# Performance work log

Measured on AMD Instinct MI355X. Metric: run time of the kernel, lower is better.

The kernel has to match this reference:

```python
import jax, jax.numpy as jnp
import numpy as np

B, L, D, H, E, V, TCAP = 64, 196, 512, 512, 512, 32000, 32


def setup_inputs() -> dict:
    key = jax.random.key(0)
    ks = jax.random.split(key, 12)
    s = 0.02  # small init scale for numerical stability
    return {
        "img_features": jax.random.normal(ks[0], (B, L, D), jnp.float32),
        "captions": jax.random.randint(ks[1], (B, TCAP), 0, V, jnp.int32),
        "embed_table": jax.random.normal(ks[2], (V, E), jnp.float32) * s,
        "W_feat": jax.random.normal(ks[3], (D, D), jnp.float32) * s,
        "W_h": jax.random.normal(ks[4], (H, D), jnp.float32) * s,
        "att_bias": jnp.zeros((L,), jnp.float32),
        "v_att": jax.random.normal(ks[5], (D,), jnp.float32) * s,
        "W_ih": jax.random.normal(ks[6], (4 * H, E + D), jnp.float32) * s,
        "W_hh": jax.random.normal(ks[7], (4 * H, H), jnp.float32) * s,
        "b_ih": jnp.zeros((4 * H,), jnp.float32),
        "b_hh": jnp.zeros((4 * H,), jnp.float32),
        "W_out": jax.random.normal(ks[8], (V, H), jnp.float32) * s,
        "b_out": jnp.zeros((V,), jnp.float32),
    }


def reference(img_features, captions, embed_table, W_feat, W_h, att_bias, v_att,
              W_ih, W_hh, b_ih, b_hh, W_out, b_out):
    # init states: mean over feature locations (D == H branch of initialize_states)
    mean_feat = img_features.mean(axis=1)            # [B, H]
    h0 = mean_feat
    c0 = mean_feat

    max_cap_len = captions.shape[1] - 1              # T
    word_emb = embed_table[captions]                 # [B, T+1, E] (no dropout: eval)
    emb_seq = jnp.swapaxes(word_emb[:, :max_cap_len, :], 0, 1)  # [T, B, E]

    # feature projection is h-independent -> hoist out of the loop
    feat_proj = jnp.einsum('bld,de->ble', img_features, W_feat)  # [B, L, D]

    def step(carry, emb_t):
        h, c = carry
        # Bahdanau attention: relu(W_feat f + W_h h + b) . v, softmax over L
        att = jax.nn.relu(feat_proj + (h @ W_h)[:, None, :] + att_bias[None, :, None])
        score = jnp.einsum('bld,d->bl', att, v_att)              # [B, L]
        alpha = jax.nn.softmax(score, axis=1)                    # [B, L]
        context = jnp.einsum('bl,bld->bd', alpha, img_features)  # [B, D]
        # LSTMCell (torch gate order: i, f, g, o)
        x = jnp.concatenate([emb_t, context], axis=1)            # [B, E+D]
        gates = x @ W_ih.T + b_ih + h @ W_hh.T + b_hh            # [B, 4H]
        i, f, g, o = jnp.split(gates, 4, axis=1)
        c_new = jax.nn.sigmoid(f) * c + jax.nn.sigmoid(i) * jnp.tanh(g)
        h_new = jax.nn.sigmoid(o) * jnp.tanh(c_new)
        out = h_new @ W_out.T + b_out                            # [B, V]
        return (h_new, c_new), (out, alpha)

    (_, _), (preds, alphas) = jax.lax.scan(step, (h0, c0), emb_seq)
    predictions = jnp.swapaxes(preds, 0, 1)   # [B, T, V]
    alphas = jnp.swapaxes(alphas, 0, 1)       # [B, T, L]
    return predictions, alphas
```

## Files before the change

### kernel.cpp

```cpp
#include <hip/hip_runtime.h>

typedef unsigned short u16;
typedef __attribute__((ext_vector_type(4))) float f32x4;
typedef __attribute__((ext_vector_type(8))) short short8;

#define B_ 64
#define L_ 196
#define D_ 512
#define T_ 31
#define V_ 32000

__device__ __forceinline__ float b2f(unsigned int u) {
    union { float f; unsigned int u; } x; x.u = u << 16; return x.f;
}
__device__ __forceinline__ u16 f2b(float f) {
    union { float f; unsigned int u; } x; x.f = f;
    unsigned int r = x.u + 0x7fffu + ((x.u >> 16) & 1u);
    return (u16)(r >> 16);
}
__device__ __forceinline__ void unpack8(uint4 v, float* f) {
    f[0] = b2f(v.x & 0xffffu); f[1] = b2f(v.x >> 16);
    f[2] = b2f(v.y & 0xffffu); f[3] = b2f(v.y >> 16);
    f[4] = b2f(v.z & 0xffffu); f[5] = b2f(v.z >> 16);
    f[6] = b2f(v.w & 0xffffu); f[7] = b2f(v.w >> 16);
}

__global__ __launch_bounds__(256) void convert_kernel(
        const float* __restrict__ src, u16* __restrict__ dst, int n4) {
    int i = blockIdx.x * 256 + threadIdx.x;
    if (i >= n4) return;
    float4 v = *(const float4*)(src + (size_t)i * 4);
    u16* d = dst + (size_t)i * 4;
    d[0] = f2b(v.x); d[1] = f2b(v.y); d[2] = f2b(v.z); d[3] = f2b(v.w);
}

__global__ __launch_bounds__(256) void prep_kernel(
        const float* __restrict__ Wfeat, const float* __restrict__ Wih,
        const float* __restrict__ Whh, const float* __restrict__ table,
        const int* __restrict__ cap,
        u16* __restrict__ WfT, u16* __restrict__ Wcat,
        u16* __restrict__ Wemb, u16* __restrict__ Aemb) {
    int idx = blockIdx.x * 256 + threadIdx.x;
    if (idx < 512 * 512) {
        WfT[idx] = f2b(Wfeat[(idx & 511) * 512 + (idx >> 9)]);
    }
    if (idx < 2048 * 1024) {
        int j = idx >> 10, k = idx & 1023;
        Wcat[idx] = f2b((k < 512) ? Wih[j * 1024 + 512 + k] : Whh[j * 512 + (k - 512)]);
    }
    if (idx < 2048 * 512) {
        int j = idx >> 9, k = idx & 511;
        Wemb[idx] = f2b(Wih[j * 1024 + k]);
    }
    if (idx < 1984 * 512) {
        int m = idx >> 9, k = idx & 511;
        int t = m >> 6, b = m & 63;
        Aemb[idx] = f2b(table[(size_t)cap[b * 32 + t] * 512 + k]);
    }
}

__global__ __launch_bounds__(512) void init_kernel(
        const float* __restrict__ img, const float* __restrict__ Wh,
        float* __restrict__ c, u16* __restrict__ xcat, float* __restrict__ hWh) {
    __shared__ float hl[512];
    int b = blockIdx.x, d = threadIdx.x;
    const float* p = img + (size_t)b * L_ * D_ + d;
    float s = 0.f;
    for (int l = 0; l < L_; l++) s += p[l * D_];
    float mean = s * (1.0f / 196.0f);
    c[b * 512 + d] = mean;
    xcat[b * 1024 + 512 + d] = f2b(mean);
    hl[d] = mean;
    __syncthreads();
    float acc = 0.f;
    const float* wp = Wh + d;
    for (int k = 0; k < 512; k++) acc += hl[k] * wp[k * 512];
    hWh[b * 512 + d] = acc;
}

__global__ __launch_bounds__(256) void score_kernel(
        const u16* __restrict__ fp, const float* __restrict__ hWh,
        const float* __restrict__ att_bias, const float* __restrict__ v_att,
        float* __restrict__ score) {
    int b = blockIdx.y;
    int l = blockIdx.x * 4 + (threadIdx.x >> 6);
    int lane = threadIdx.x & 63;
    uint4 fv = *(const uint4*)(fp + ((size_t)(b * L_ + l)) * D_ + lane * 8);
    float4 h0 = *(const float4*)(hWh + b * D_ + lane * 8);
    float4 h1 = *(const float4*)(hWh + b * D_ + lane * 8 + 4);
    float4 v0 = *(const float4*)(v_att + lane * 8);
    float4 v1 = *(const float4*)(v_att + lane * 8 + 4);
    float ab = att_bias[l];
    float f[8];
    unpack8(fv, f);
    float hh[8] = {h0.x, h0.y, h0.z, h0.w, h1.x, h1.y, h1.z, h1.w};
    float vv[8] = {v0.x, v0.y, v0.z, v0.w, v1.x, v1.y, v1.z, v1.w};
    float acc = 0.f;
#pragma unroll
    for (int j = 0; j < 8; j++) {
        float a = f[j] + hh[j] + ab;
        a = fmaxf(a, 0.f);
        acc += a * vv[j];
    }
#pragma unroll
    for (int off = 32; off; off >>= 1) acc += __shfl_xor(acc, off, 64);
    if (lane == 0) score[b * L_ + l] = acc;
}

__global__ __launch_bounds__(256) void softctx_kernel(
        const float* __restrict__ score, const float* __restrict__ img,
        float* __restrict__ alphas_out, u16* __restrict__ xcat, int t) {
    __shared__ float sl[256];
    __shared__ float al[196];
    int b = blockIdx.x, tid = threadIdx.x;
    float s = (tid < L_) ? score[b * L_ + tid] : -3.4e38f;
    sl[tid] = s;
    __syncthreads();
    for (int off = 128; off; off >>= 1) {
        if (tid < off) sl[tid] = fmaxf(sl[tid], sl[tid + off]);
        __syncthreads();
    }
    float mx = sl[0];
    __syncthreads();
    float e = (tid < L_) ? expf(s - mx) : 0.f;
    sl[tid] = e;
    __syncthreads();
    for (int off = 128; off; off >>= 1) {
        if (tid < off) sl[tid] += sl[tid + off];
        __syncthreads();
    }
    float inv = 1.f / sl[0];
    if (tid < L_) {
        float a = e * inv;
        al[tid] = a;
        alphas_out[((size_t)(b * T_ + t)) * L_ + tid] = a;
    }
    __syncthreads();
    float c0 = 0.f, c1 = 0.f;
    const float* ib = img + (size_t)b * L_ * D_;
    for (int l = 0; l < L_; l++) {
        float a = al[l];
        c0 += a * ib[l * D_ + tid];
        c1 += a * ib[l * D_ + tid + 256];
    }
    xcat[b * 1024 + tid] = f2b(c0);
    xcat[b * 1024 + tid + 256] = f2b(c1);
}

__global__ __launch_bounds__(256) void gates_kernel(
        const u16* __restrict__ xcat, const u16* __restrict__ Wcat,
        const float* __restrict__ gemb, const float* __restrict__ bih,
        const float* __restrict__ bhh, float* __restrict__ gates, int t) {
    __shared__ __align__(16) u16 At[16 * 40];
    __shared__ __align__(16) u16 Bt[64 * 40];
    int tid = threadIdx.x, wave = tid >> 6, lane = tid & 63;
    int m0 = blockIdx.y * 16, n0 = blockIdx.x * 64;
    f32x4 acc = {0.f, 0.f, 0.f, 0.f};
    int sr = tid >> 2, sc = (tid & 3) * 8;
    const u16* Ap = xcat + (size_t)(m0 + (sr & 15)) * 1024 + sc;
    const u16* Bp = Wcat + (size_t)(n0 + sr) * 1024 + sc;
    int fm = lane & 15, fk = (lane >> 4) * 8;
    for (int k0 = 0; k0 < 1024; k0 += 32) {
        uint4 av = {0, 0, 0, 0};
        uint4 bv = *(const uint4*)(Bp + k0);
        if (tid < 64) av = *(const uint4*)(Ap + k0);
        __syncthreads();
        if (tid < 64) *(uint4*)(&At[(sr & 15) * 40 + sc]) = av;
        *(uint4*)(&Bt[sr * 40 + sc]) = bv;
        __syncthreads();
        short8 a = *(const short8*)(&At[fm * 40 + fk]);
        short8 bb = *(const short8*)(&Bt[(wave * 16 + fm) * 40 + fk]);
        acc = __builtin_amdgcn_mfma_f32_16x16x32_bf16(a, bb, acc, 0, 0, 0);
    }
    int crow = (lane >> 4) * 4, ccol = n0 + wave * 16 + (lane & 15);
#pragma unroll
    for (int r = 0; r < 4; r++) {
        int row = m0 + crow + r;
        float v = acc[r] + gemb[((size_t)(t * 64 + row)) * 2048 + ccol]
                + bih[ccol] + bhh[ccol];
        gates[row * 2048 + ccol] = v;
    }
}

__global__ __launch_bounds__(512) void lstm_kernel(
        const float* __restrict__ gates, float* __restrict__ c,
        const float* __restrict__ Wh, u16* __restrict__ xcat,
        u16* __restrict__ hseq, float* __restrict__ hWh, int t) {
    __shared__ float hl[512];
    int b = blockIdx.x, d = threadIdx.x;
    const float* g = gates + b * 2048;
    float gi = g[d], gf = g[512 + d], gg = g[1024 + d], go = g[1536 + d];
    float cold = c[b * 512 + d];
    float si = 1.f / (1.f + expf(-gi));
    float sf = 1.f / (1.f + expf(-gf));
    float so = 1.f / (1.f + expf(-go));
    float cn = sf * cold + si * tanhf(gg);
    float hn = so * tanhf(cn);
    c[b * 512 + d] = cn;
    u16 hb = f2b(hn);
    xcat[b * 1024 + 512 + d] = hb;
    hseq[((size_t)(b * T_ + t)) * 512 + d] = hb;
    hl[d] = hn;
    __syncthreads();
    float acc = 0.f;
    const float* wp = Wh + d;
    for (int k = 0; k < 512; k++) acc += hl[k] * wp[k * 512];
    hWh[b * 512 + d] = acc;
}

template <int MODE>
__global__ __launch_bounds__(256) void gemm64_kernel(
        const u16* __restrict__ A, const u16* __restrict__ Bm,
        int lda, int ldb, int K, void* __restrict__ Cv, int ldc,
        const float* __restrict__ bias) {
    __shared__ __align__(16) u16 At[64 * 40];
    __shared__ __align__(16) u16 Bt[64 * 40];
    int tid = threadIdx.x, wave = tid >> 6, lane = tid & 63;
    int wm = (wave >> 1) * 32, wn = (wave & 1) * 32;
    size_t m0 = (size_t)blockIdx.y * 64, n0 = (size_t)blockIdx.x * 64;
    f32x4 acc[2][2];
#pragma unroll
    for (int i = 0; i < 2; i++)
#pragma unroll
        for (int j = 0; j < 2; j++) acc[i][j] = {0.f, 0.f, 0.f, 0.f};
    int sr = tid >> 2, sc = (tid & 3) * 8;
    const u16* Ap = A + (m0 + sr) * (size_t)lda + sc;
    const u16* Bp = Bm + (n0 + sr) * (size_t)ldb + sc;
    int fm = lane & 15, fk = (lane >> 4) * 8;
    for (int k0 = 0; k0 < K; k0 += 32) {
        uint4 av = *(const uint4*)(Ap + k0);
        uint4 bv = *(const uint4*)(Bp + k0);
        __syncthreads();
        *(uint4*)(&At[sr * 40 + sc]) = av;
        *(uint4*)(&Bt[sr * 40 + sc]) = bv;
        __syncthreads();
        short8 a0 = *(const short8*)(&At[(wm + fm) * 40 + fk]);
        short8 a1 = *(const short8*)(&At[(wm + 16 + fm) * 40 + fk]);
        short8 b0 = *(const short8*)(&Bt[(wn + fm) * 40 + fk]);
        short8 b1 = *(const short8*)(&Bt[(wn + 16 + fm) * 40 + fk]);
        acc[0][0] = __builtin_amdgcn_mfma_f32_16x16x32_bf16(a0, b0, acc[0][0], 0, 0, 0);
        acc[0][1] = __builtin_amdgcn_mfma_f32_16x16x32_bf16(a0, b1, acc[0][1], 0, 0, 0);
        acc[1][0] = __builtin_amdgcn_mfma_f32_16x16x32_bf16(a1, b0, acc[1][0], 0, 0, 0);
        acc[1][1] = __builtin_amdgcn_mfma_f32_16x16x32_bf16(a1, b1, acc[1][1], 0, 0, 0);
    }
    int crow = (lane >> 4) * 4, ccol = lane & 15;
#pragma unroll
    for (int mi = 0; mi < 2; mi++)
#pragma unroll
        for (int ni = 0; ni < 2; ni++)
#pragma unroll
            for (int r = 0; r < 4; r++) {
                size_t row = m0 + wm + mi * 16 + crow + r;
                size_t col = n0 + wn + ni * 16 + ccol;
                float v = acc[mi][ni][r];
                if (MODE == 0) {
                    ((u16*)Cv)[row * (size_t)ldc + col] = f2b(v);
                } else {
                    if (MODE == 1) v += bias[col];
                    ((float*)Cv)[row * (size_t)ldc + col] = v;
                }
            }
}

extern "C" void kernel_launch(void* const* d_in, const int* in_sizes, int n_in,
                              void* d_out, int out_size, void* d_ws, size_t ws_size,
                              hipStream_t stream) {
    (void)in_sizes; (void)n_in; (void)out_size; (void)ws_size;
    const float* img   = (const float*)d_in[0];
    const int*   cap   = (const int*)d_in[1];
    const float* table = (const float*)d_in[2];
    const float* Wf    = (const float*)d_in[3];
    const float* Wh    = (const float*)d_in[4];
    const float* ab    = (const float*)d_in[5];
    const float* va    = (const float*)d_in[6];
    const float* Wih   = (const float*)d_in[7];
    const float* Whh   = (const float*)d_in[8];
    const float* bih   = (const float*)d_in[9];
    const float* bhh   = (const float*)d_in[10];
    const float* Wout  = (const float*)d_in[11];
    const float* bout  = (const float*)d_in[12];

    float* dout = (float*)d_out;
    float* alph = dout + (size_t)B_ * T_ * V_;

    char* w = (char*)d_ws;
    u16*   imgb  = (u16*)(w);
    u16*   fpb   = (u16*)(w + 12845056);
    u16*   Woutb = (u16*)(w + 25690112);
    u16*   Wcat  = (u16*)(w + 58458112);
    u16*   Wemb  = (u16*)(w + 62652416);
    u16*   WfT   = (u16*)(w + 64749568);
    u16*   Aemb  = (u16*)(w + 65273856);
    u16*   hseq  = (u16*)(w + 67305472);
    float* gemb  = (float*)(w + 69337088);
    u16*   xcat  = (u16*)(w + 85590016);
    float* gates = (float*)(w + 85721088);
    float* score = (float*)(w + 86245376);
    float* hWh   = (float*)(w + 86295552);
    float* cbuf  = (float*)(w + 86426624);

    convert_kernel<<<6272, 256, 0, stream>>>(img, imgb, 12544 * 512 / 4);
    convert_kernel<<<16000, 256, 0, stream>>>(Wout, Woutb, 32000 * 512 / 4);
    prep_kernel<<<8192, 256, 0, stream>>>(Wf, Wih, Whh, table, cap, WfT, Wcat, Wemb, Aemb);
    gemm64_kernel<0><<<dim3(8, 196), 256, 0, stream>>>(imgb, WfT, 512, 512, 512, fpb, 512, nullptr);
    gemm64_kernel<2><<<dim3(32, 31), 256, 0, stream>>>(Aemb, Wemb, 512, 512, 512, gemb, 2048, nullptr);
    init_kernel<<<64, 512, 0, stream>>>(img, Wh, cbuf, xcat, hWh);

    for (int t = 0; t < T_; t++) {
        score_kernel<<<dim3(49, 64), 256, 0, stream>>>(fpb, hWh, ab, va, score);
        softctx_kernel<<<64, 256, 0, stream>>>(score, img, alph, xcat, t);
        gates_kernel<<<dim3(32, 4), 256, 0, stream>>>(xcat, Wcat, gemb, bih, bhh, gates, t);
        lstm_kernel<<<64, 512, 0, stream>>>(gates, cbuf, Wh, xcat, hseq, hWh, t);
    }

    gemm64_kernel<1><<<dim3(500, 31), 256, 0, stream>>>(hseq, Woutb, 512, 512, 512, dout, 32000, bout);
}
```

Baseline: 1.907 ms.

## Fuse recurrent timestep kernels into one persistent cooperative kernel with grid syncs

Replaces the four per-timestep kernel launches (score, softmax/context, gates GEMM, LSTM) with a single cooperative persistent kernel of 256 blocks that uses grid.sync between phases. Each phase is re-partitioned across more blocks, with split-K partial sums for the gates and split-D for context and the hWh projection, and the cell state is double-buffered. The intent is to remove launch overhead and idle GPU time across 124 tiny launches in exchange for grid-barrier cost. It also adds an XCD-aware block swizzle and nontemporal stores to the output-projection GEMM.

Measured after the change: 4.884 ms. 156% more time.

```diff
diff --git a/kernel.cpp b/kernel.cpp
--- a/kernel.cpp
+++ b/kernel.cpp
@@ -1,4 +1,7 @@
 #include <hip/hip_runtime.h>
+#include <hip/hip_cooperative_groups.h>
+
+namespace cg = cooperative_groups;
 
 typedef unsigned short u16;
 typedef __attribute__((ext_vector_type(4))) float f32x4;
@@ -78,137 +81,180 @@
     hWh[b * 512 + d] = acc;
 }
 
-__global__ __launch_bounds__(256) void score_kernel(
-        const u16* __restrict__ fp, const float* __restrict__ hWh,
-        const float* __restrict__ att_bias, const float* __restrict__ v_att,
-        float* __restrict__ score) {
-    int b = blockIdx.y;
-    int l = blockIdx.x * 4 + (threadIdx.x >> 6);
-    int lane = threadIdx.x & 63;
-    uint4 fv = *(const uint4*)(fp + ((size_t)(b * L_ + l)) * D_ + lane * 8);
-    float4 h0 = *(const float4*)(hWh + b * D_ + lane * 8);
-    float4 h1 = *(const float4*)(hWh + b * D_ + lane * 8 + 4);
-    float4 v0 = *(const float4*)(v_att + lane * 8);
-    float4 v1 = *(const float4*)(v_att + lane * 8 + 4);
-    float ab = att_bias[l];
-    float f[8];
-    unpack8(fv, f);
-    float hh[8] = {h0.x, h0.y, h0.z, h0.w, h1.x, h1.y, h1.z, h1.w};
-    float vv[8] = {v0.x, v0.y, v0.z, v0.w, v1.x, v1.y, v1.z, v1.w};
-    float acc = 0.f;
-#pragma unroll
-    for (int j = 0; j < 8; j++) {
-        float a = f[j] + hh[j] + ab;
-        a = fmaxf(a, 0.f);
-        acc += a * vv[j];
-    }
-#pragma unroll
-    for (int off = 32; off; off >>= 1) acc += __shfl_xor(acc, off, 64);
-    if (lane == 0) score[b * L_ + l] = acc;
-}
-
-__global__ __launch_bounds__(256) void softctx_kernel(
-        const float* __restrict__ score, const float* __restrict__ img,
-        float* __restrict__ alphas_out, u16* __restrict__ xcat, int t) {
+__global__ __launch_bounds__(512, 2) void loop_kernel(
+        const float* __restrict__ img,
+        const u16*   __restrict__ fpb,
+        const float* __restrict__ Wh,
+        const float* __restrict__ ab,
+        const float* __restrict__ va,
+        const u16*   __restrict__ Wcat,
+        const float* __restrict__ gemb,
+        const float* __restrict__ bih, const float* __restrict__ bhh,
+        u16*   __restrict__ xcat,
+        u16*   __restrict__ hseq,
+        float* __restrict__ score,
+        float* __restrict__ hWh,
+        float* __restrict__ c0b, float* __restrict__ c1b,
+        float* __restrict__ gpart,
+        float* __restrict__ alph) {
+    __shared__ __align__(16) u16 At[64 * 40];
+    __shared__ __align__(16) u16 Bt[64 * 40];
+    __shared__ float hl[512];
+    __shared__ float fbuf[512];
     __shared__ float sl[256];
     __shared__ float al[196];
-    int b = blockIdx.x, tid = threadIdx.x;
-    float s = (tid < L_) ? score[b * L_ + tid] : -3.4e38f;
-    sl[tid] = s;
-    __syncthreads();
-    for (int off = 128; off; off >>= 1) {
-        if (tid < off) sl[tid] = fmaxf(sl[tid], sl[tid + off]);
-        __syncthreads();
-    }
-    float mx = sl[0];
-    __syncthreads();
-    float e = (tid < L_) ? expf(s - mx) : 0.f;
-    sl[tid] = e;
-    __syncthreads();
-    for (int off = 128; off; off >>= 1) {
-        if (tid < off) sl[tid] += sl[tid + off];
-        __syncthreads();
-    }
-    float inv = 1.f / sl[0];
-    if (tid < L_) {
-        float a = e * inv;
-        al[tid] = a;
-        alphas_out[((size_t)(b * T_ + t)) * L_ + tid] = a;
-    }
-    __syncthreads();
-    float c0 = 0.f, c1 = 0.f;
-    const float* ib = img + (size_t)b * L_ * D_;
-    for (int l = 0; l < L_; l++) {
-        float a = al[l];
-        c0 += a * ib[l * D_ + tid];
-        c1 += a * ib[l * D_ + tid + 256];
-    }
-    xcat[b * 1024 + tid] = f2b(c0);
-    xcat[b * 1024 + tid + 256] = f2b(c1);
-}
-
-__global__ __launch_bounds__(256) void gates_kernel(
-        const u16* __restrict__ xcat, const u16* __restrict__ Wcat,
-        const float* __restrict__ gemb, const float* __restrict__ bih,
-        const float* __restrict__ bhh, float* __restrict__ gates, int t) {
-    __shared__ __align__(16) u16 At[16 * 40];
-    __shared__ __align__(16) u16 Bt[64 * 40];
-    int tid = threadIdx.x, wave = tid >> 6, lane = tid & 63;
-    int m0 = blockIdx.y * 16, n0 = blockIdx.x * 64;
-    f32x4 acc = {0.f, 0.f, 0.f, 0.f};
-    int sr = tid >> 2, sc = (tid & 3) * 8;
-    const u16* Ap = xcat + (size_t)(m0 + (sr & 15)) * 1024 + sc;
-    const u16* Bp = Wcat + (size_t)(n0 + sr) * 1024 + sc;
-    int fm = lane & 15, fk = (lane >> 4) * 8;
-    for (int k0 = 0; k0 < 1024; k0 += 32) {
-        uint4 av = {0, 0, 0, 0};
-        uint4 bv = *(const uint4*)(Bp + k0);
-        if (tid < 64) av = *(const uint4*)(Ap + k0);
-        __syncthreads();
-        if (tid < 64) *(uint4*)(&At[(sr & 15) * 40 + sc]) = av;
-        *(uint4*)(&Bt[sr * 40 + sc]) = bv;
-        __syncthreads();
-        short8 a = *(const short8*)(&At[fm * 40 + fk]);
-        short8 bb = *(const short8*)(&Bt[(wave * 16 + fm) * 40 + fk]);
-        acc = __builtin_amdgcn_mfma_f32_16x16x32_bf16(a, bb, acc, 0, 0, 0);
-    }
-    int crow = (lane >> 4) * 4, ccol = n0 + wave * 16 + (lane & 15);
-#pragma unroll
-    for (int r = 0; r < 4; r++) {
-        int row = m0 + crow + r;
-        float v = acc[r] + gemb[((size_t)(t * 64 + row)) * 2048 + ccol]
-                + bih[ccol] + bhh[ccol];
-        gates[row * 2048 + ccol] = v;
-    }
-}
-
-__global__ __launch_bounds__(512) void lstm_kernel(
-        const float* __restrict__ gates, float* __restrict__ c,
-        const float* __restrict__ Wh, u16* __restrict__ xcat,
-        u16* __restrict__ hseq, float* __restrict__ hWh, int t) {
-    __shared__ float hl[512];
-    int b = blockIdx.x, d = threadIdx.x;
-    const float* g = gates + b * 2048;
-    float gi = g[d], gf = g[512 + d], gg = g[1024 + d], go = g[1536 + d];
-    float cold = c[b * 512 + d];
-    float si = 1.f / (1.f + expf(-gi));
-    float sf = 1.f / (1.f + expf(-gf));
-    float so = 1.f / (1.f + expf(-go));
-    float cn = sf * cold + si * tanhf(gg);
-    float hn = so * tanhf(cn);
-    c[b * 512 + d] = cn;
-    u16 hb = f2b(hn);
-    xcat[b * 1024 + 512 + d] = hb;
-    hseq[((size_t)(b * T_ + t)) * 512 + d] = hb;
-    hl[d] = hn;
-    __syncthreads();
-    float acc = 0.f;
-    const float* wp = Wh + d;
-    for (int k = 0; k < 512; k++) acc += hl[k] * wp[k * 512];
-    hWh[b * 512 + d] = acc;
-}
-
-template <int MODE>
+
+    cg::grid_group grid = cg::this_grid();
+    int bid = blockIdx.x;
+    int tid = threadIdx.x;
+    int lane = tid & 63;
+    int wv = tid >> 6;
+
+    for (int t = 0; t < T_; t++) {
+        {
+            int gw = bid * 8 + wv;
+            int b = gw >> 5;
+            int lw = gw & 31;
+            float4 h0 = *(const float4*)(hWh + b * 512 + lane * 8);
+            float4 h1 = *(const float4*)(hWh + b * 512 + lane * 8 + 4);
+            float4 v0 = *(const float4*)(va + lane * 8);
+            float4 v1 = *(const float4*)(va + lane * 8 + 4);
+            float hh[8] = {h0.x, h0.y, h0.z, h0.w, h1.x, h1.y, h1.z, h1.w};
+            float vv[8] = {v0.x, v0.y, v0.z, v0.w, v1.x, v1.y, v1.z, v1.w};
+            for (int l = lw; l < L_; l += 32) {
+                uint4 fv = *(const uint4*)(fpb + ((size_t)(b * L_ + l)) * 512 + lane * 8);
+                float f[8];
+                unpack8(fv, f);
+                float abl = ab[l];
+                float acc = 0.f;
+#pragma unroll
+                for (int j = 0; j < 8; j++) {
+                    float a = f[j] + hh[j] + abl;
+                    a = fmaxf(a, 0.f);
+                    acc += a * vv[j];
+                }
+#pragma unroll
+                for (int off = 32; off; off >>= 1) acc += __shfl_xor(acc, off, 64);
+                if (lane == 0) score[b * L_ + l] = acc;
+            }
+        }
+        grid.sync();
+        {
+            int b = bid >> 2, q = bid & 3;
+            float s = (tid < L_) ? score[b * L_ + tid] : -3.4e38f;
+            if (tid < 256) sl[tid] = s;
+            __syncthreads();
+            for (int off = 128; off; off >>= 1) {
+                if (tid < off) sl[tid] = fmaxf(sl[tid], sl[tid + off]);
+                __syncthreads();
+            }
+            float mx = sl[0];
+            __syncthreads();
+            float e = (tid < L_) ? expf(s - mx) : 0.f;
+            if (tid < 256) sl[tid] = e;
+            __syncthreads();
+            for (int off = 128; off; off >>= 1) {
+                if (tid < off) sl[tid] += sl[tid + off];
+                __syncthreads();
+            }
+            float inv = 1.f / sl[0];
+            if (tid < L_) {
+                float a = e * inv;
+                al[tid] = a;
+                if (q == 0) alph[((size_t)(b * T_ + t)) * L_ + tid] = a;
+            }
+            __syncthreads();
+            int dq = tid & 127, ls = tid >> 7;
+            const float* ib = img + (size_t)b * L_ * 512 + q * 128 + dq;
+            float cacc = 0.f;
+            for (int l = ls; l < L_; l += 4) cacc += al[l] * ib[(size_t)l * 512];
+            fbuf[tid] = cacc;
+            __syncthreads();
+            if (tid < 128) {
+                float v = fbuf[tid] + fbuf[tid + 128] + fbuf[tid + 256] + fbuf[tid + 384];
+                xcat[b * 1024 + q * 128 + tid] = f2b(v);
+            }
+        }
+        grid.sync();
+        {
+            int nt = bid >> 3, p = bid & 7;
+            int sr = tid >> 3, sc4 = (tid & 7) * 4;
+            const u16* Ap = xcat + sr * 1024 + p * 128 + sc4;
+            const u16* Bp = Wcat + ((size_t)(nt * 64 + sr)) * 1024 + p * 128 + sc4;
+            int mi = wv & 3, nj = wv >> 2;
+            int fm = lane & 15, fk = (lane >> 4) * 8;
+            f32x4 a0 = {0.f, 0.f, 0.f, 0.f}, a1 = {0.f, 0.f, 0.f, 0.f};
+            for (int k0 = 0; k0 < 128; k0 += 32) {
+                uint2 av = *(const uint2*)(Ap + k0);
+                uint2 bv = *(const uint2*)(Bp + k0);
+                __syncthreads();
+                *(uint2*)(&At[sr * 40 + sc4]) = av;
+                *(uint2*)(&Bt[sr * 40 + sc4]) = bv;
+                __syncthreads();
+                short8 af = *(const short8*)(&At[(mi * 16 + fm) * 40 + fk]);
+                short8 b0 = *(const short8*)(&Bt[(nj * 32 + fm) * 40 + fk]);
+                short8 b1 = *(const short8*)(&Bt[(nj * 32 + 16 + fm) * 40 + fk]);
+                a0 = __builtin_amdgcn_mfma_f32_16x16x32_bf16(af, b0, a0, 0, 0, 0);
+                a1 = __builtin_amdgcn_mfma_f32_16x16x32_bf16(af, b1, a1, 0, 0, 0);
+            }
+            int crow = (lane >> 4) * 4, ccol = lane & 15;
+            float* gp = gpart + (size_t)p * 64 * 2048;
+#pragma unroll
+            for (int r = 0; r < 4; r++) {
+                int row = mi * 16 + crow + r;
+                int col = nt * 64 + nj * 32 + ccol;
+                gp[row * 2048 + col] = a0[r];
+                gp[row * 2048 + col + 16] = a1[r];
+            }
+        }
+        grid.sync();
+        {
+            int b = bid >> 2, q = bid & 3;
+            const float* cin = (t & 1) ? c1b : c0b;
+            float* cout      = (t & 1) ? c0b : c1b;
+            int d = tid;
+            float gi = 0.f, gf = 0.f, gg = 0.f, go = 0.f;
+#pragma unroll
+            for (int p = 0; p < 8; p++) {
+                const float* gp = gpart + (size_t)(p * 64 + b) * 2048;
+                gi += gp[d]; gf += gp[512 + d]; gg += gp[1024 + d]; go += gp[1536 + d];
+            }
+            const float* ge = gemb + ((size_t)(t * 64 + b)) * 2048;
+            gi += ge[d]        + bih[d]        + bhh[d];
+            gf += ge[512 + d]  + bih[512 + d]  + bhh[512 + d];
+            gg += ge[1024 + d] + bih[1024 + d] + bhh[1024 + d];
+            go += ge[1536 + d] + bih[1536 + d] + bhh[1536 + d];
+            float cold = cin[b * 512 + d];
+            float si = 1.f / (1.f + expf(-gi));
+            float sf = 1.f / (1.f + expf(-gf));
+            float so = 1.f / (1.f + expf(-go));
+            float cn = sf * cold + si * tanhf(gg);
+            float hn = so * tanhf(cn);
+            if (q == 0) {
+                cout[b * 512 + d] = cn;
+                u16 hb = f2b(hn);
+                xcat[b * 1024 + 512 + d] = hb;
+                hseq[((size_t)(b * T_ + t)) * 512 + d] = hb;
+            }
+            hl[d] = hn;
+            __syncthreads();
+            int dq = q * 128 + (tid & 127);
+            int kbase = (tid >> 7) * 128;
+            const float* wp = Wh + dq;
+            float acc = 0.f;
+#pragma unroll 8
+            for (int k = 0; k < 128; k++) acc += hl[kbase + k] * wp[(size_t)(kbase + k) * 512];
+            fbuf[tid] = acc;
+            __syncthreads();
+            if (tid < 128)
+                hWh[b * 512 + q * 128 + tid] =
+                    fbuf[tid] + fbuf[tid + 128] + fbuf[tid + 256] + fbuf[tid + 384];
+        }
+        grid.sync();
+    }
+}
+
+template <int MODE, int SWZ>
 __global__ __launch_bounds__(256) void gemm64_kernel(
         const u16* __restrict__ A, const u16* __restrict__ Bm,
         int lda, int ldb, int K, void* __restrict__ Cv, int ldc,
@@ -217,7 +263,17 @@
     __shared__ __align__(16) u16 Bt[64 * 40];
     int tid = threadIdx.x, wave = tid >> 6, lane = tid & 63;
     int wm = (wave >> 1) * 32, wn = (wave & 1) * 32;
-    size_t m0 = (size_t)blockIdx.y * 64, n0 = (size_t)blockIdx.x * 64;
+    size_t m0, n0;
+    if (SWZ) {
+        unsigned lin = blockIdx.y * gridDim.x + blockIdx.x;
+        const unsigned q = 15500u / 8u, r = 15500u % 8u;
+        unsigned xcd = lin & 7u, pos = lin >> 3;
+        unsigned wg = (xcd < r ? xcd * (q + 1u) : r * (q + 1u) + (xcd - r) * q) + pos;
+        unsigned mt = wg % 31u, nt = wg / 31u;
+        m0 = (size_t)mt * 64; n0 = (size_t)nt * 64;
+    } else {
+        m0 = (size_t)blockIdx.y * 64; n0 = (size_t)blockIdx.x * 64;
+    }
     f32x4 acc[2][2];
 #pragma unroll
     for (int i = 0; i < 2; i++)
@@ -255,8 +311,10 @@
                 float v = acc[mi][ni][r];
                 if (MODE == 0) {
                     ((u16*)Cv)[row * (size_t)ldc + col] = f2b(v);
+                } else if (MODE == 1) {
+                    v += bias[col];
+                    __builtin_nontemporal_store(v, (float*)Cv + row * (size_t)ldc + col);
                 } else {
-                    if (MODE == 1) v += bias[col];
                     ((float*)Cv)[row * (size_t)ldc + col] = v;
                 }
             }
@@ -294,24 +352,35 @@
     u16*   hseq  = (u16*)(w + 67305472);
     float* gemb  = (float*)(w + 69337088);
     u16*   xcat  = (u16*)(w + 85590016);
-    float* gates = (float*)(w + 85721088);
-    float* score = (float*)(w + 86245376);
-    float* hWh   = (float*)(w + 86295552);
-    float* cbuf  = (float*)(w + 86426624);
+    float* score = (float*)(w + 85721088);
+    float* hWh   = (float*)(w + 85771264);
+    float* cbuf0 = (float*)(w + 85902336);
+    float* cbuf1 = (float*)(w + 86033408);
+    float* gpart = (float*)(w + 86164480);
 
     convert_kernel<<<6272, 256, 0, stream>>>(img, imgb, 12544 * 512 / 4);
     convert_kernel<<<16000, 256, 0, stream>>>(Wout, Woutb, 32000 * 512 / 4);
     prep_kernel<<<8192, 256, 0, stream>>>(Wf, Wih, Whh, table, cap, WfT, Wcat, Wemb, Aemb);
-    gemm64_kernel<0><<<dim3(8, 196), 256, 0, stream>>>(imgb, WfT, 512, 512, 512, fpb, 512, nullptr);
-    gemm64_kernel<2><<<dim3(32, 31), 256, 0, stream>>>(Aemb, Wemb, 512, 512, 512, gemb, 2048, nullptr);
-    init_kernel<<<64, 512, 0, stream>>>(img, Wh, cbuf, xcat, hWh);
-
-    for (int t = 0; t < T_; t++) {
-        score_kernel<<<dim3(49, 64), 256, 0, stream>>>(fpb, hWh, ab, va, score);
-        softctx_kernel<<<64, 256, 0, stream>>>(score, img, alph, xcat, t);
-        gates_kernel<<<dim3(32, 4), 256, 0, stream>>>(xcat, Wcat, gemb, bih, bhh, gates, t);
-        lstm_kernel<<<64, 512, 0, stream>>>(gates, cbuf, Wh, xcat, hseq, hWh, t);
-    }
-
-    gemm64_kernel<1><<<dim3(500, 31), 256, 0, stream>>>(hseq, Woutb, 512, 512, 512, dout, 32000, bout);
-}
+    gemm64_kernel<0, 0><<<dim3(8, 196), 256, 0, stream>>>(imgb, WfT, 512, 512, 512, fpb, 512, nullptr);
+    gemm64_kernel<2, 0><<<dim3(32, 31), 256, 0, stream>>>(Aemb, Wemb, 512, 512, 512, gemb, 2048, nullptr);
+    init_kernel<<<64, 512, 0, stream>>>(img, Wh, cbuf0, xcat, hWh);
+
+    {
+        const float* a_img = img;  const u16* a_fpb = fpb;  const float* a_Wh = Wh;
+        const float* a_ab = ab;    const float* a_va = va;  const u16* a_Wcat = Wcat;
+        const float* a_gemb = gemb; const float* a_bih = bih; const float* a_bhh = bhh;
+        u16* a_xcat = xcat; u16* a_hseq = hseq; float* a_score = score;
+        float* a_hWh = hWh; float* a_c0 = cbuf0; float* a_c1 = cbuf1;
+        float* a_gp = gpart; float* a_al = alph;
+        void* args[] = {
+            (void*)&a_img, (void*)&a_fpb, (void*)&a_Wh, (void*)&a_ab, (void*)&a_va,
+            (void*)&a_Wcat, (void*)&a_gemb, (void*)&a_bih, (void*)&a_bhh,
+            (void*)&a_xcat, (void*)&a_hseq, (void*)&a_score, (void*)&a_hWh,
+            (void*)&a_c0, (void*)&a_c1, (void*)&a_gp, (void*)&a_al
+        };
+        hipLaunchCooperativeKernel((const void*)loop_kernel, dim3(256), dim3(512),
+                                   args, 0, stream);
+    }
+
+    gemm64_kernel<1, 1><<<dim3(500, 31), 256, 0, stream>>>(hseq, Woutb, 512, 512, 512, dout, 32000, bout);
+}
```
